# Optimization experiments

Measured on AMD Instinct MI355X. Metric: run time of the kernel, lower is better.

## Reference

```python
import jax, jax.numpy as jnp
import numpy as np


def _conv1x1_relu(x, W, b):
    # x: (B, Cin, N, k), W: (Cout, Cin), b: (Cout,) -> (B, Cout, N, k)
    return jax.nn.relu(jnp.einsum('bcnk,oc->bonk', x, W) + b[None, :, None, None])


def _knn_idx(pc, k):
    # pc: (B, C, N). Mirrors torch: dis_mat = -||pi - pj||^2, topk (largest) -> nearest.
    G = jnp.einsum('bcn,bcm->bnm', pc, pc)            # (B, N, N)
    sq = jnp.sum(pc * pc, axis=1)                      # (B, N)
    neg_dist = 2.0 * G - sq[:, :, None] - sq[:, None, :]
    _, idx = jax.lax.top_k(neg_dist, k)                # (B, N, k) int32
    return idx


def _group_points(x, idx):
    # x: (B, C, N), idx: (B, N, k) -> (B, C, N, k); out[b,c,n,j] = x[b,c,idx[b,n,j]]
    B, C, N = x.shape
    k = idx.shape[-1]
    idx2 = jnp.broadcast_to(idx.reshape(B, 1, N * k), (B, C, N * k))
    return jnp.take_along_axis(x, idx2, axis=2).reshape(B, C, N, k)


def setup_inputs() -> dict:
    key = jax.random.key(0)
    ks = jax.random.split(key, 8)
    B, N, C, O, K = 8, 4096, 64, 64, 16
    s = 0.05
    return {
        'xyz': jax.random.normal(ks[0], (B, 3, N), dtype=jnp.float32),
        'fea': jax.random.normal(ks[1], (B, C, N), dtype=jnp.float32),
        'Wg1': jax.random.normal(ks[2], (O, 10), dtype=jnp.float32) * s,
        'bg1': jnp.zeros((O,), dtype=jnp.float32),
        'Wg2': jax.random.normal(ks[3], (O, O), dtype=jnp.float32) * s,
        'bg2': jnp.zeros((O,), dtype=jnp.float32),
        'Wf1': jax.random.normal(ks[4], (O, 2 * C), dtype=jnp.float32) * s,
        'bf1': jnp.zeros((O,), dtype=jnp.float32),
        'Wf2': jax.random.normal(ks[5], (O, O), dtype=jnp.float32) * s,
        'bf2': jnp.zeros((O,), dtype=jnp.float32),
        'Wf3': jax.random.normal(ks[6], (O, O), dtype=jnp.float32) * s,
        'bf3': jnp.zeros((O,), dtype=jnp.float32),
        'k': 16,
    }


def reference(xyz, fea, Wg1, bg1, Wg2, bg2, Wf1, bf1, Wf2, bf2, Wf3, bf3, k):
    idx = _knn_idx(fea, k)                             # (B, N, k)

    # get_edge_point: (B, 10, N, k)
    xyz_knn = _group_points(xyz, idx)                  # (B, 3, N, k)
    xyz_c = jnp.broadcast_to(xyz[:, :, :, None], xyz_knn.shape)
    xyz_r = xyz_c - xyz_knn
    xyz_d = jnp.sqrt(jnp.sum(xyz_r * xyz_r, axis=1, keepdims=True))
    geo = jnp.concatenate([xyz_d, xyz_c, xyz_knn, xyz_r], axis=1)

    # get_edge_feature: (B, 2C, N, k)
    fea_knn = _group_points(fea, idx)
    fea_c = jnp.broadcast_to(fea[:, :, :, None], fea_knn.shape)
    edge = jnp.concatenate([fea_c, fea_knn], axis=1)

    g = _conv1x1_relu(geo, Wg1, bg1)
    g = _conv1x1_relu(g, Wg2, bg2)

    f = _conv1x1_relu(edge, Wf1, bf1)
    f = _conv1x1_relu(f, Wf2, bf2)
    f = _conv1x1_relu(f, Wf3, bf3)

    out = jnp.max(g * f, axis=-1)                      # (B, O, N)
    return out
```

## Files before the change

### kernel.cpp

```cpp
#include <hip/hip_runtime.h>
#include <math.h>

#define NB 8
#define NPTS 4096
#define NCH 64
#define NOUT 64
#define KNN 16

#define GLOBAL_AS const __attribute__((address_space(1)))
#define LDS_AS __attribute__((address_space(3)))

#define WS_SQ  0
#define WS_PT  (NB*NPTS)
#define WS_QT  (WS_PT + NB*NPTS*64)
#define WS_IDX (WS_QT + NB*NPTS*64)

__global__ __launch_bounds__(256) void k_sq(const float* __restrict__ fea,
                                            float* __restrict__ sq) {
    int g = blockIdx.x * 256 + threadIdx.x;
    int b = g >> 12, n = g & 4095;
    const float* f = fea + (size_t)b * NCH * NPTS + n;
    float s = 0.f;
#pragma unroll
    for (int c = 0; c < NCH; ++c) s = fmaf(f[c * NPTS], f[c * NPTS], s);
    sq[g] = s;
}

__global__ __launch_bounds__(256, 2) void k_knn(const float* __restrict__ fea,
                                                const float* __restrict__ sq,
                                                int* __restrict__ idxout) {
    __shared__ __align__(16) float rowT[64][64];
    __shared__ __align__(16) float colT[2][64 * 64];

    const int b = blockIdx.y;
    const int n0 = blockIdx.x * 64;
    const int tid = threadIdx.x;
    const int lane = tid & 63, w = tid >> 6;
    const int g = lane >> 4, p = lane & 15;
    const int rbase = w * 16 + g * 4;
    const float* feab = fea + (size_t)b * NCH * NPTS;

    auto stage_async = [&](int buf, int m0) {
#pragma unroll
        for (int i = 0; i < 4; ++i) {
            int k = w * 4 + i;
            int c = 4 * k + (lane >> 4);
            int j = (lane & 15) * 4;
            const float* gp = feab + c * NPTS + m0 + j;
            float* lp = &colT[buf][k * 256];
            __builtin_amdgcn_global_load_lds((GLOBAL_AS void*)gp,
                                             (LDS_AS void*)lp, 16, 0, 0);
        }
    };

#pragma unroll
    for (int i = 0; i < 4; ++i) {
        int e = i * 1024 + tid * 4;
        int c = e >> 6, r = e & 63;
        *(float4*)&rowT[c][r] = *(const float4*)&feab[c * NPTS + n0 + r];
    }
    stage_async(0, 0);

    float lstv[4];
    int   lsti[4];
#pragma unroll
    for (int i = 0; i < 4; ++i) { lstv[i] = -3.0e38f; lsti[i] = 0; }

    auto ins = [&](int i, float vv, int col) {
        unsigned long long lt = __ballot(lstv[i] < vv);
        int pos = __popc((unsigned)((lt >> (g * 16)) & 0xFFFFull));
        float nv = __shfl_down(lstv[i], 1, 16);
        int   ni = __shfl_down(lsti[i], 1, 16);
        if (p <= pos - 2)      { lstv[i] = nv; lsti[i] = ni; }
        else if (p == pos - 1) { lstv[i] = vv; lsti[i] = col; }
    };

    __syncthreads();

    for (int t = 0; t < 64; ++t) {
        const int m0 = t * 64;
        const int cur = t & 1;
        if (t < 63) stage_async(cur ^ 1, m0 + 64);

        float4 sqc = *(const float4*)&sq[b * NPTS + m0 + p * 4];

        float acc[4][4] = {{0.f,0.f,0.f,0.f},{0.f,0.f,0.f,0.f},
                           {0.f,0.f,0.f,0.f},{0.f,0.f,0.f,0.f}};
#pragma unroll 8
        for (int c = 0; c < 64; ++c) {
            float4 rv = *(const float4*)&rowT[c][rbase];
            float4 cv = *(const float4*)&colT[cur][c * 64 + p * 4];
            float rr[4] = {rv.x, rv.y, rv.z, rv.w};
            float cc[4] = {cv.x, cv.y, cv.z, cv.w};
#pragma unroll
            for (int ri = 0; ri < 4; ++ri)
#pragma unroll
                for (int ci = 0; ci < 4; ++ci)
                    acc[ri][ci] = fmaf(rr[ri], cc[ci], acc[ri][ci]);
        }

        float thr[4];
#pragma unroll
        for (int i = 0; i < 4; ++i) {
            acc[i][0] = 2.f * acc[i][0] - sqc.x;
            acc[i][1] = 2.f * acc[i][1] - sqc.y;
            acc[i][2] = 2.f * acc[i][2] - sqc.z;
            acc[i][3] = 2.f * acc[i][3] - sqc.w;
            thr[i] = __shfl(lstv[i], 0, 16);
        }

#pragma unroll
        for (int i = 0; i < 4; ++i) {
            float vm = fmaxf(fmaxf(acc[i][0], acc[i][1]),
                             fmaxf(acc[i][2], acc[i][3]));
            unsigned long long bal = __ballot(vm > thr[i]);
            unsigned mg = (unsigned)((bal >> (g * 16)) & 0xFFFFull);
            while (__any(mg != 0u)) {
                bool act = (mg != 0u);
                int srcp = act ? (__ffs(mg) - 1) : 0;
                mg &= (mg - 1u);
                int srcl = (g << 4) | srcp;
                float c0 = __shfl(acc[i][0], srcl);
                float c1 = __shfl(acc[i][1], srcl);
                float c2 = __shfl(acc[i][2], srcl);
                float c3 = __shfl(acc[i][3], srcl);
                if (act) {
                    int cb = m0 + srcp * 4;
                    if (c0 > thr[i]) ins(i, c0, cb + 0);
                    if (c1 > thr[i]) ins(i, c1, cb + 1);
                    if (c2 > thr[i]) ins(i, c2, cb + 2);
                    if (c3 > thr[i]) ins(i, c3, cb + 3);
                }
            }
        }
        __syncthreads();
    }

#pragma unroll
    for (int i = 0; i < 4; ++i) {
        int row = rbase + i;
        idxout[((size_t)(b * NPTS) + n0 + row) * KNN + (15 - p)] = lsti[i];
    }
}

__global__ __launch_bounds__(256) void k_pq(const float* __restrict__ fea,
                                            const float* __restrict__ Wf1,
                                            const float* __restrict__ bf1,
                                            float* __restrict__ Pt,
                                            float* __restrict__ Qt) {
    __shared__ __align__(16) float feaT[64][64];
    __shared__ __align__(16) float WT[64][132];
    __shared__ float sb[64];

    const int b = blockIdx.y;
    const int n0 = blockIdx.x * 64;
    const int tid = threadIdx.x;
    const int to = tid & 15, tn = tid >> 4;
    const float* feab = fea + (size_t)b * NCH * NPTS;

#pragma unroll
    for (int i = 0; i < 4; ++i) {
        int e = i * 1024 + tid * 4;
        int c = e >> 6, nn = e & 63;
        *(float4*)&feaT[c][nn] = *(const float4*)&feab[c * NPTS + n0 + nn];
    }
#pragma unroll
    for (int i = 0; i < 8; ++i) {
        int g = tid * 32 + i * 4;
        int op = g >> 6, c = g & 63;
        const float* src = (op < 64) ? &Wf1[op * 128 + c]
                                     : &Wf1[(op - 64) * 128 + 64 + c];
        float4 w = *(const float4*)src;
        WT[c + 0][op] = w.x; WT[c + 1][op] = w.y;
        WT[c + 2][op] = w.z; WT[c + 3][op] = w.w;
    }
    if (tid < 64) sb[tid] = bf1[tid];
    __syncthreads();

    float acc[4][8];
#pragma unroll
    for (int ni = 0; ni < 4; ++ni)
#pragma unroll
        for (int oj = 0; oj < 8; ++oj) acc[ni][oj] = 0.f;

#pragma unroll 4
    for (int c = 0; c < 64; ++c) {
        float4 a  = *(const float4*)&feaT[c][tn * 4];
        float4 w0 = *(const float4*)&WT[c][to * 8];
        float4 w1 = *(const float4*)&WT[c][to * 8 + 4];
        float av[4] = {a.x, a.y, a.z, a.w};
        float wv[8] = {w0.x, w0.y, w0.z, w0.w, w1.x, w1.y, w1.z, w1.w};
#pragma unroll
        for (int ni = 0; ni < 4; ++ni)
#pragma unroll
            for (int oj = 0; oj < 8; ++oj)
                acc[ni][oj] = fmaf(av[ni], wv[oj], acc[ni][oj]);
    }

    const int opb = to * 8;
#pragma unroll
    for (int ni = 0; ni < 4; ++ni) {
        int n = n0 + tn * 4 + ni;
        size_t base = ((size_t)b * NPTS + n) * 64;
        if (opb < 64) {
            float4 o0, o1;
            o0.x = acc[ni][0] + sb[opb + 0]; o0.y = acc[ni][1] + sb[opb + 1];
            o0.z = acc[ni][2] + sb[opb + 2]; o0.w = acc[ni][3] + sb[opb + 3];
            o1.x = acc[ni][4] + sb[opb + 4]; o1.y = acc[ni][5] + sb[opb + 5];
            o1.z = acc[ni][6] + sb[opb + 6]; o1.w = acc[ni][7] + sb[opb + 7];
            *(float4*)&Pt[base + opb]     = o0;
            *(float4*)&Pt[base + opb + 4] = o1;
        } else {
            float4 o0, o1;
            o0.x = acc[ni][0]; o0.y = acc[ni][1]; o0.z = acc[ni][2]; o0.w = acc[ni][3];
            o1.x = acc[ni][4]; o1.y = acc[ni][5]; o1.z = acc[ni][6]; o1.w = acc[ni][7];
            *(float4*)&Qt[base + opb - 64]     = o0;
            *(float4*)&Qt[base + opb - 64 + 4] = o1;
        }
    }
}

__global__ __launch_bounds__(256) void k_mlp(
    const float* __restrict__ xyz,
    const float* __restrict__ Pt, const float* __restrict__ Qt,
    const int* __restrict__ knnidx,
    const float* __restrict__ Wg1, const float* __restrict__ bg1,
    const float* __restrict__ Wg2, const float* __restrict__ bg2,
    const float* __restrict__ Wf2, const float* __restrict__ bf2,
    const float* __restrict__ Wf3, const float* __restrict__ bf3,
    float* __restrict__ out) {
    __shared__ __align__(16) float bufX[64][68];
    __shared__ __align__(16) float bufY[64][68];
    __shared__ __align__(16) float Wbuf[64][68];
    __shared__ __align__(16) float scratch[1280];
    __shared__ float biasS[64];
    __shared__ int sidx[64];

    const int b = blockIdx.y;
    const int n0 = blockIdx.x * 4;
    const int tid = threadIdx.x;
    const int to = tid & 15, tp = tid >> 4;

    if (tid < 64)
        sidx[tid] = knnidx[((size_t)(b * NPTS + n0)) * KNN + tid];
    __syncthreads();

    {
        int pair = tid >> 2, q = tid & 3;
        int m = sidx[pair];
        int pt = pair >> 4;
        const float* pB = &Pt[((size_t)b * NPTS + n0 + pt) * 64];
        const float* qB = &Qt[((size_t)b * NPTS + m) * 64];
#pragma unroll
        for (int i = 0; i < 4; ++i) {
            int c0 = q * 16 + i * 4;
            float4 pv = *(const float4*)&pB[c0];
            float4 qv = *(const float4*)&qB[c0];
            bufX[c0 + 0][pair] = fmaxf(pv.x + qv.x, 0.f);
            bufX[c0 + 1][pair] = fmaxf(pv.y + qv.y, 0.f);
            bufX[c0 + 2][pair] = fmaxf(pv.z + qv.z, 0.f);
            bufX[c0 + 3][pair] = fmaxf(pv.w + qv.w, 0.f);
        }
    }
    if (tid < 64) {
        int pair = tid, pt = pair >> 4;
        int m = sidx[pair];
        const float* xb = xyz + (size_t)b * 3 * NPTS;
        float cx = xb[0 * NPTS + n0 + pt], cy = xb[1 * NPTS + n0 + pt], cz = xb[2 * NPTS + n0 + pt];
        float kx = xb[0 * NPTS + m], ky = xb[1 * NPTS + m], kz = xb[2 * NPTS + m];
        float rx = cx - kx, ry = cy - ky, rz = cz - kz;
        float d = sqrtf(rx * rx + ry * ry + rz * rz);
        scratch[0 * 68 + pair] = d;
        scratch[1 * 68 + pair] = cx; scratch[2 * 68 + pair] = cy; scratch[3 * 68 + pair] = cz;
        scratch[4 * 68 + pair] = kx; scratch[5 * 68 + pair] = ky; scratch[6 * 68 + pair] = kz;
        scratch[7 * 68 + pair] = rx; scratch[8 * 68 + pair] = ry; scratch[9 * 68 + pair] = rz;
    }

    auto stageW = [&](const float* W, const float* bv) {
#pragma unroll
        for (int i = 0; i < 4; ++i) {
            int g = tid * 16 + i * 4;
            int o = g >> 6, c = g & 63;
            float4 w = *(const float4*)&W[g];
            Wbuf[c + 0][o] = w.x; Wbuf[c + 1][o] = w.y;
            Wbuf[c + 2][o] = w.z; Wbuf[c + 3][o] = w.w;
        }
        if (tid < 64) biasS[tid] = bv[tid];
    };

    auto gemmPh = [&](const float* src, float* dst, int Kdim) {
        float acc[4][4] = {{0.f,0.f,0.f,0.f},{0.f,0.f,0.f,0.f},
                           {0.f,0.f,0.f,0.f},{0.f,0.f,0.f,0.f}};
#pragma unroll 2
        for (int c = 0; c < Kdim; ++c) {
            float4 w = *(const float4*)&Wbuf[c][to * 4];
            float4 a = *(const float4*)(src + c * 68 + tp * 4);
            float wr[4] = {w.x, w.y, w.z, w.w};
            float ar[4] = {a.x, a.y, a.z, a.w};
#pragma unroll
            for (int oi = 0; oi < 4; ++oi)
#pragma unroll
                for (int pj = 0; pj < 4; ++pj)
                    acc[oi][pj] = fmaf(wr[oi], ar[pj], acc[oi][pj]);
        }
#pragma unroll
        for (int oi = 0; oi < 4; ++oi) {
            float bo = biasS[to * 4 + oi];
            float4 o4;
            o4.x = fmaxf(acc[oi][0] + bo, 0.f);
            o4.y = fmaxf(acc[oi][1] + bo, 0.f);
            o4.z = fmaxf(acc[oi][2] + bo, 0.f);
            o4.w = fmaxf(acc[oi][3] + bo, 0.f);
            *(float4*)(dst + (to * 4 + oi) * 68 + tp * 4) = o4;
        }
    };

    stageW(Wf2, bf2);
    __syncthreads();
    gemmPh(&bufX[0][0], &bufY[0][0], 64);
    __syncthreads();
    stageW(Wf3, bf3);
    __syncthreads();
    gemmPh(&bufY[0][0], &bufX[0][0], 64);
    __syncthreads();
    {
        for (int e = tid; e < 640; e += 256) {
            int o = e / 10, c = e - o * 10;
            Wbuf[c][o] = Wg1[e];
        }
        if (tid < 64) biasS[tid] = bg1[tid];
    }
    __syncthreads();
    gemmPh(scratch, &bufY[0][0], 10);
    __syncthreads();
    stageW(Wg2, bg2);
    __syncthreads();
    {
        float acc[4][4] = {{0.f,0.f,0.f,0.f},{0.f,0.f,0.f,0.f},
                           {0.f,0.f,0.f,0.f},{0.f,0.f,0.f,0.f}};
#pragma unroll 2
        for (int c = 0; c < 64; ++c) {
            float4 w = *(const float4*)&Wbuf[c][to * 4];
            float4 a = *(const float4*)&bufY[c][tp * 4];
            float wr[4] = {w.x, w.y, w.z, w.w};
            float ar[4] = {a.x, a.y, a.z, a.w};
#pragma unroll
            for (int oi = 0; oi < 4; ++oi)
#pragma unroll
                for (int pj = 0; pj < 4; ++pj)
                    acc[oi][pj] = fmaf(wr[oi], ar[pj], acc[oi][pj]);
        }
#pragma unroll
        for (int oi = 0; oi < 4; ++oi) {
            int o = to * 4 + oi;
            float bo = biasS[o];
            float mx = -3.0e38f;
#pragma unroll
            for (int pj = 0; pj < 4; ++pj) {
                float g2v = fmaxf(acc[oi][pj] + bo, 0.f);
                float f3v = bufX[o][tp * 4 + pj];
                mx = fmaxf(mx, g2v * f3v);
            }
            scratch[o * 17 + tp] = mx;
        }
    }
    __syncthreads();
    {
        int o = tid & 63, pt = tid >> 6;
        float m0_ = scratch[o * 17 + pt * 4 + 0];
        float m1  = scratch[o * 17 + pt * 4 + 1];
        float m2  = scratch[o * 17 + pt * 4 + 2];
        float m3  = scratch[o * 17 + pt * 4 + 3];
        out[((size_t)b * 64 + o) * NPTS + n0 + pt] =
            fmaxf(fmaxf(m0_, m1), fmaxf(m2, m3));
    }
}

extern "C" void kernel_launch(void* const* d_in, const int* in_sizes, int n_in,
                              void* d_out, int out_size, void* d_ws, size_t ws_size,
                              hipStream_t stream) {
    const float* xyz = (const float*)d_in[0];
    const float* fea = (const float*)d_in[1];
    const float* Wg1 = (const float*)d_in[2];
    const float* bg1 = (const float*)d_in[3];
    const float* Wg2 = (const float*)d_in[4];
    const float* bg2 = (const float*)d_in[5];
    const float* Wf1 = (const float*)d_in[6];
    const float* bf1 = (const float*)d_in[7];
    const float* Wf2 = (const float*)d_in[8];
    const float* bf2 = (const float*)d_in[9];
    const float* Wf3 = (const float*)d_in[10];
    const float* bf3 = (const float*)d_in[11];
    float* out = (float*)d_out;
    float* ws = (float*)d_ws;

    float* sq = ws + WS_SQ;
    float* Pt = ws + WS_PT;
    float* Qt = ws + WS_QT;
    int* idxw = (int*)(ws + WS_IDX);

    k_sq <<<dim3(128),      dim3(256), 0, stream>>>(fea, sq);
    k_knn<<<dim3(64, 8),    dim3(256), 0, stream>>>(fea, sq, idxw);
    k_pq <<<dim3(64, 8),    dim3(256), 0, stream>>>(fea, Wf1, bf1, Pt, Qt);
    k_mlp<<<dim3(1024, 8),  dim3(256), 0, stream>>>(xyz, Pt, Qt, idxw,
                                                    Wg1, bg1, Wg2, bg2,
                                                    Wf2, bf2, Wf3, bf3, out);
}
```

Before: 737.1 us.

## Widen KNN column tile to 128 and refresh threshold after each half

The KNN distance kernel now processes 128 candidate columns per iteration instead of 64. Each thread computes a 4x8 register tile, which reuses each row LDS load across twice as many FMAs and halves the number of barriers and loop iterations. The top-k threshold is now carried across iterations and refreshed only after a half-tile produced insertions. LDS use grows to 80KB per block and register pressure rises, which may lower occupancy under launch_bounds(256,2).

After: 734.7 us. Within noise of the previous version (-0.3%).

```diff
diff --git a/kernel.cpp b/kernel.cpp
--- a/kernel.cpp
+++ b/kernel.cpp
@@ -30,7 +30,7 @@
                                                 const float* __restrict__ sq,
                                                 int* __restrict__ idxout) {
     __shared__ __align__(16) float rowT[64][64];
-    __shared__ __align__(16) float colT[2][64 * 64];
+    __shared__ __align__(16) float colT[2][64 * 128];
 
     const int b = blockIdx.y;
     const int n0 = blockIdx.x * 64;
@@ -42,10 +42,10 @@
 
     auto stage_async = [&](int buf, int m0) {
 #pragma unroll
-        for (int i = 0; i < 4; ++i) {
-            int k = w * 4 + i;
-            int c = 4 * k + (lane >> 4);
-            int j = (lane & 15) * 4;
+        for (int i = 0; i < 8; ++i) {
+            int k = w * 8 + i;
+            int c = 2 * k + (lane >> 5);
+            int j = (lane & 31) * 4;
             const float* gp = feab + c * NPTS + m0 + j;
             float* lp = &colT[buf][k * 256];
             __builtin_amdgcn_global_load_lds((GLOBAL_AS void*)gp,
@@ -63,8 +63,11 @@
 
     float lstv[4];
     int   lsti[4];
-#pragma unroll
-    for (int i = 0; i < 4; ++i) { lstv[i] = -3.0e38f; lsti[i] = 0; }
+    float thr[4];
+#pragma unroll
+    for (int i = 0; i < 4; ++i) {
+        lstv[i] = -3.0e38f; lsti[i] = 0; thr[i] = -3.0e38f;
+    }
 
     auto ins = [&](int i, float vv, int col) {
         unsigned long long lt = __ballot(lstv[i] < vv);
@@ -77,60 +80,72 @@
 
     __syncthreads();
 
-    for (int t = 0; t < 64; ++t) {
-        const int m0 = t * 64;
+    for (int t = 0; t < 32; ++t) {
+        const int m0 = t * 128;
         const int cur = t & 1;
-        if (t < 63) stage_async(cur ^ 1, m0 + 64);
-
-        float4 sqc = *(const float4*)&sq[b * NPTS + m0 + p * 4];
-
-        float acc[4][4] = {{0.f,0.f,0.f,0.f},{0.f,0.f,0.f,0.f},
-                           {0.f,0.f,0.f,0.f},{0.f,0.f,0.f,0.f}};
-#pragma unroll 8
+        if (t < 31) stage_async(cur ^ 1, m0 + 128);
+
+        float4 sql = *(const float4*)&sq[b * NPTS + m0 + p * 4];
+        float4 sqh = *(const float4*)&sq[b * NPTS + m0 + 64 + p * 4];
+
+        float acc[4][8];
+#pragma unroll
+        for (int i = 0; i < 4; ++i)
+#pragma unroll
+            for (int j = 0; j < 8; ++j) acc[i][j] = 0.f;
+
+#pragma unroll 4
         for (int c = 0; c < 64; ++c) {
-            float4 rv = *(const float4*)&rowT[c][rbase];
-            float4 cv = *(const float4*)&colT[cur][c * 64 + p * 4];
+            float4 rv  = *(const float4*)&rowT[c][rbase];
+            float4 cv0 = *(const float4*)&colT[cur][c * 128 + p * 4];
+            float4 cv1 = *(const float4*)&colT[cur][c * 128 + 64 + p * 4];
             float rr[4] = {rv.x, rv.y, rv.z, rv.w};
-            float cc[4] = {cv.x, cv.y, cv.z, cv.w};
-#pragma unroll
-            for (int ri = 0; ri < 4; ++ri)
-#pragma unroll
-                for (int ci = 0; ci < 4; ++ci)
-                    acc[ri][ci] = fmaf(rr[ri], cc[ci], acc[ri][ci]);
-        }
-
-        float thr[4];
+            float c0[4] = {cv0.x, cv0.y, cv0.z, cv0.w};
+            float c1[4] = {cv1.x, cv1.y, cv1.z, cv1.w};
+#pragma unroll
+            for (int ri = 0; ri < 4; ++ri) {
+#pragma unroll
+                for (int cj = 0; cj < 4; ++cj) {
+                    acc[ri][cj]     = fmaf(rr[ri], c0[cj], acc[ri][cj]);
+                    acc[ri][cj + 4] = fmaf(rr[ri], c1[cj], acc[ri][cj + 4]);
+                }
+            }
+        }
+
+        float sqa[8] = {sql.x, sql.y, sql.z, sql.w, sqh.x, sqh.y, sqh.z, sqh.w};
+#pragma unroll
+        for (int i = 0; i < 4; ++i)
+#pragma unroll
+            for (int j = 0; j < 8; ++j)
+                acc[i][j] = fmaf(2.f, acc[i][j], -sqa[j]);
+
 #pragma unroll
         for (int i = 0; i < 4; ++i) {
-            acc[i][0] = 2.f * acc[i][0] - sqc.x;
-            acc[i][1] = 2.f * acc[i][1] - sqc.y;
-            acc[i][2] = 2.f * acc[i][2] - sqc.z;
-            acc[i][3] = 2.f * acc[i][3] - sqc.w;
-            thr[i] = __shfl(lstv[i], 0, 16);
-        }
-
-#pragma unroll
-        for (int i = 0; i < 4; ++i) {
-            float vm = fmaxf(fmaxf(acc[i][0], acc[i][1]),
-                             fmaxf(acc[i][2], acc[i][3]));
-            unsigned long long bal = __ballot(vm > thr[i]);
-            unsigned mg = (unsigned)((bal >> (g * 16)) & 0xFFFFull);
-            while (__any(mg != 0u)) {
-                bool act = (mg != 0u);
-                int srcp = act ? (__ffs(mg) - 1) : 0;
-                mg &= (mg - 1u);
-                int srcl = (g << 4) | srcp;
-                float c0 = __shfl(acc[i][0], srcl);
-                float c1 = __shfl(acc[i][1], srcl);
-                float c2 = __shfl(acc[i][2], srcl);
-                float c3 = __shfl(acc[i][3], srcl);
-                if (act) {
-                    int cb = m0 + srcp * 4;
-                    if (c0 > thr[i]) ins(i, c0, cb + 0);
-                    if (c1 > thr[i]) ins(i, c1, cb + 1);
-                    if (c2 > thr[i]) ins(i, c2, cb + 2);
-                    if (c3 > thr[i]) ins(i, c3, cb + 3);
+#pragma unroll
+            for (int h = 0; h < 2; ++h) {
+                float v0 = acc[i][h * 4 + 0], v1 = acc[i][h * 4 + 1];
+                float v2 = acc[i][h * 4 + 2], v3 = acc[i][h * 4 + 3];
+                float vm = fmaxf(fmaxf(v0, v1), fmaxf(v2, v3));
+                unsigned long long bal = __ballot(vm > thr[i]);
+                unsigned mg = (unsigned)((bal >> (g * 16)) & 0xFFFFull);
+                while (__any(mg != 0u)) {
+                    bool act = (mg != 0u);
+                    int srcp = act ? (__ffs(mg) - 1) : 0;
+                    mg &= (mg - 1u);
+                    int srcl = (g << 4) | srcp;
+                    float b0 = __shfl(v0, srcl);
+                    float b1 = __shfl(v1, srcl);
+                    float b2 = __shfl(v2, srcl);
+                    float b3 = __shfl(v3, srcl);
+                    if (act) {
+                        int cb = m0 + h * 64 + srcp * 4;
+                        if (b0 > thr[i]) ins(i, b0, cb + 0);
+                        if (b1 > thr[i]) ins(i, b1, cb + 1);
+                        if (b2 > thr[i]) ins(i, b2, cb + 2);
+                        if (b3 > thr[i]) ins(i, b3, cb + 3);
+                    }
                 }
+                if (bal) thr[i] = __shfl(lstv[i], 0, 16);
             }
         }
         __syncthreads();
```
